# Optimization experiments

Measured on AMD Instinct MI355X. Metric: run time of the kernel, lower is better.

## Reference

```python
import jax, jax.numpy as jnp
import numpy as np
import math

D_MODEL = 512
N_HEAD = 8
TAU = 0.5


def _leaky_integrate(x):
    # dx/dt = -x / tau; x + dx/dt  (with tau=0.5 this equals -x)
    return x + (-x / TAU)


def setup_inputs() -> dict:
    key = jax.random.key(0)
    ks = jax.random.split(key, 12)
    B, S, D = 4, 2048, D_MODEL
    s = 1.0 / math.sqrt(D)
    inp = {
        "query": jax.random.normal(ks[0], (B, S, D), jnp.float32),
        "key": jax.random.normal(ks[1], (B, S, D), jnp.float32),
        "value": jax.random.normal(ks[2], (B, S, D), jnp.float32),
        "Wq": jax.random.normal(ks[3], (D, D), jnp.float32) * s,
        "bq": jnp.zeros((D,), jnp.float32),
        "Wk": jax.random.normal(ks[4], (D, D), jnp.float32) * s,
        "bk": jnp.zeros((D,), jnp.float32),
        "Wv": jax.random.normal(ks[5], (D, D), jnp.float32) * s,
        "bv": jnp.zeros((D,), jnp.float32),
        "Wo": jax.random.normal(ks[6], (D, D), jnp.float32) * s,
        "bo": jnp.zeros((D,), jnp.float32),
    }
    return inp


def reference(query, key, value, Wq, bq, Wk, bk, Wv, bv, Wo, bo):
    B, S, D = query.shape
    H = N_HEAD
    dh = D // H
    # linear projections (torch Linear: x @ W^T + b)
    q = query @ Wq.T + bq
    k = key @ Wk.T + bk
    v = value @ Wv.T + bv
    # (B, S, D) -> (B, H, S, dh)
    q = q.reshape(B, S, H, dh).transpose(0, 2, 1, 3)
    k = k.reshape(B, S, H, dh).transpose(0, 2, 1, 3)
    v = v.reshape(B, S, H, dh).transpose(0, 2, 1, 3)
    # leaky integration on q, k
    q = _leaky_integrate(q)
    k = _leaky_integrate(k)
    # scores scaled by sqrt(d_model) (NOT head dim) per the source
    scores = jnp.einsum("bhsd,bhtd->bhst", q, k) / math.sqrt(D_MODEL)
    attn = jax.nn.softmax(scores, axis=-1)
    # conductance-based synapse: elementwise sigmoid AFTER softmax
    attn = jax.nn.sigmoid(attn)
    out = jnp.einsum("bhst,bhtd->bhsd", attn, v)
    out = out.transpose(0, 2, 1, 3).reshape(B, S, D)
    return out @ Wo.T + bo
```

## Files before the change

kernel.cpp:

```cpp
#include <hip/hip_runtime.h>
#include <stdint.h>
#include <math.h>

using u16    = unsigned short;
using short8 = __attribute__((ext_vector_type(8))) short;
using f32x4  = __attribute__((ext_vector_type(4))) float;
using f32x16 = __attribute__((ext_vector_type(16))) float;
using u32x4  = __attribute__((ext_vector_type(4))) uint32_t;

#define DEVI __device__ __forceinline__
#define FENCE asm volatile("" ::: "memory")
#define GPTR(p) ((const __attribute__((address_space(1))) uint32_t*)(p))
#define LPTR(p) ((__attribute__((address_space(3))) uint32_t*)(p))

static constexpr int S  = 2048;
static constexpr int D  = 512;
static constexpr int DH = 64;
static constexpr float C2 = 0.063763906f;

DEVI u16 f2bf(float f){
  uint32_t u = __float_as_uint(f);
  u = u + 0x7FFFu + ((u >> 16) & 1u);
  return (u16)(u >> 16);
}

DEVI uint32_t cvt_pk_bf16(float a, float b){
  uint32_t d;
  asm("v_cvt_pk_bf16_f32 %0, %1, %2" : "=v"(d) : "v"(a), "v"(b));
  return d;
}

__global__ void k_cvt3(const float* __restrict__ a, const float* __restrict__ b,
                       const float* __restrict__ c, u16* __restrict__ out){
  int i = blockIdx.x * blockDim.x + threadIdx.x;
  const float* src = (i < (1<<20)) ? a : (i < (2<<20) ? b : c);
  float4 v = reinterpret_cast<const float4*>(src)[i & ((1<<20)-1)];
  uint2 o;
  o.x = (uint32_t)f2bf(v.x) | ((uint32_t)f2bf(v.y) << 16);
  o.y = (uint32_t)f2bf(v.z) | ((uint32_t)f2bf(v.w) << 16);
  reinterpret_cast<uint2*>(out)[i] = o;
}

__global__ void k_cvtw(const float* __restrict__ a, const float* __restrict__ b,
                       const float* __restrict__ c, const float* __restrict__ d,
                       u16* __restrict__ out){
  int i = blockIdx.x * blockDim.x + threadIdx.x;
  int sel = i >> 16;
  const float* src = sel == 0 ? a : sel == 1 ? b : sel == 2 ? c : d;
  float4 v = reinterpret_cast<const float4*>(src)[i & ((1<<16)-1)];
  uint2 o;
  o.x = (uint32_t)f2bf(v.x) | ((uint32_t)f2bf(v.y) << 16);
  o.y = (uint32_t)f2bf(v.z) | ((uint32_t)f2bf(v.w) << 16);
  reinterpret_cast<uint2*>(out)[i] = o;
}

template<int MODE>
__global__ __launch_bounds__(512)
void k_gemm_bt(const u16* __restrict__ A, const u16* __restrict__ W,
               const float* __restrict__ bias, void* __restrict__ outp, float oscale)
{
  __shared__ __align__(16) u16 As[2][128*64];
  __shared__ __align__(16) u16 Bs[2][128*64];
  const int tid = threadIdx.x;
  const int w = tid >> 6, l = tid & 63;
  const int wm = w & 3, wn = w >> 2;
  const int m0 = blockIdx.x * 128, n0 = blockIdx.y * 128;
  const int srow = l >> 3, sslot = l & 7;

  f32x4 acc[2][4];
  #pragma unroll
  for (int i = 0; i < 2; i++)
    #pragma unroll
    for (int j = 0; j < 4; j++)
      #pragma unroll
      for (int r = 0; r < 4; r++) acc[i][j][r] = 0.f;

  auto STAGE = [&](int buf, int kt){
    #pragma unroll
    for (int i = 0; i < 2; i++){
      int r = w*16 + i*8 + srow;
      int scol = (sslot ^ (r & 7)) * 8;
      long ga;
      if constexpr (MODE == 3){
        int m = m0 + r, k = kt + scol;
        ga = ((long)(((m >> 11)*8 + (k >> 6))*2048 + (m & 2047)))*64 + (k & 63);
      } else {
        ga = (long)(m0 + r)*D + kt + scol;
      }
      __builtin_amdgcn_global_load_lds(GPTR(A + ga), LPTR(&As[buf][(w*16 + i*8)*64]), 16, 0, 0);
      long gb = (long)(n0 + r)*D + kt + scol;
      __builtin_amdgcn_global_load_lds(GPTR(W + gb), LPTR(&Bs[buf][(w*16 + i*8)*64]), 16, 0, 0);
    }
  };

  STAGE(0, 0);
  asm volatile("s_waitcnt vmcnt(0)" ::: "memory");
  __builtin_amdgcn_s_barrier();
  FENCE;

  for (int kt = 0; kt < D; kt += 64){
    int buf = (kt >> 6) & 1;
    if (kt + 64 < D) STAGE(buf ^ 1, kt + 64);
    #pragma unroll
    for (int ks = 0; ks < 2; ks++){
      short8 af[2];
      #pragma unroll
      for (int mf = 0; mf < 2; mf++){
        int row = wm*32 + mf*16 + (l & 15);
        int cw = (ks*4 + (l >> 4)) ^ (row & 7);
        af[mf] = *reinterpret_cast<const short8*>(&As[buf][(row*8 + cw)*8]);
      }
      #pragma unroll
      for (int nf = 0; nf < 4; nf++){
        int row = wn*64 + nf*16 + (l & 15);
        int cw = (ks*4 + (l >> 4)) ^ (row & 7);
        short8 bf = *reinterpret_cast<const short8*>(&Bs[buf][(row*8 + cw)*8]);
        #pragma unroll
        for (int mf = 0; mf < 2; mf++)
          acc[mf][nf] = __builtin_amdgcn_mfma_f32_16x16x32_bf16(af[mf], bf, acc[mf][nf], 0, 0, 0);
      }
    }
    asm volatile("s_waitcnt vmcnt(0)" ::: "memory");
    __builtin_amdgcn_s_barrier();
    FENCE;
  }

  #pragma unroll
  for (int mf = 0; mf < 2; mf++){
    #pragma unroll
    for (int nf = 0; nf < 4; nf++){
      int n = n0 + wn*64 + nf*16 + (l & 15);
      float bi;
      if constexpr (MODE == 3) bi = bias[(m0 >> 11)*512 + n];
      else                     bi = bias[n];
      if constexpr (MODE == 2){
        int mb = m0 + wm*32 + mf*16 + (l >> 4)*4;
        int b_ = mb >> 11, s_ = mb & 2047;
        int h_ = n >> 6, d_ = n & 63;
        uint2 o;
        o.x = (uint32_t)f2bf((acc[mf][nf][0] + bi)*oscale) | ((uint32_t)f2bf((acc[mf][nf][1] + bi)*oscale) << 16);
        o.y = (uint32_t)f2bf((acc[mf][nf][2] + bi)*oscale) | ((uint32_t)f2bf((acc[mf][nf][3] + bi)*oscale) << 16);
        *reinterpret_cast<uint2*>(&((u16*)outp)[((long)((b_*8 + h_)*64 + d_))*2048 + s_]) = o;
      } else {
        #pragma unroll
        for (int r = 0; r < 4; r++){
          int m = m0 + wm*32 + mf*16 + (l >> 4)*4 + r;
          float v = (acc[mf][nf][r] + bi)*oscale;
          if constexpr (MODE == 3){
            ((float*)outp)[(long)m*D + n] = v;
          } else {
            int b_ = m >> 11, s_ = m & 2047;
            int h_ = n >> 6, d_ = n & 63;
            ((u16*)outp)[((long)((b_*8 + h_)*2048 + s_))*64 + d_] = f2bf(v);
          }
        }
      }
    }
  }
}

__global__ __launch_bounds__(256)
void k_sumv(const u16* __restrict__ Vt, float* __restrict__ SV){
  const int w = threadIdx.x >> 6, l = threadIdx.x & 63;
  const int row = blockIdx.x*4 + w;
  const u16* src = Vt + (long)row * S;
  float s = 0.f;
  #pragma unroll
  for (int j = 0; j < 4; j++){
    short8 v = *reinterpret_cast<const short8*>(&src[j*512 + l*8]);
    #pragma unroll
    for (int e = 0; e < 8; e++)
      s += __uint_as_float(((uint32_t)(u16)v[e]) << 16);
  }
  #pragma unroll
  for (int m = 1; m < 64; m <<= 1) s += __shfl_xor(s, m, 64);
  if (l == 0) SV[row] = s;
}

__global__ __launch_bounds__(256)
void k_bias2(const float* __restrict__ SV, const float* __restrict__ Wo,
             const float* __restrict__ bo, float* __restrict__ bias2){
  const int w = threadIdx.x >> 6, l = threadIdx.x & 63;
  const int idx = blockIdx.x*4 + w;
  const int b = idx >> 9, n = idx & 511;
  float dot = 0.f;
  #pragma unroll
  for (int j = 0; j < 2; j++){
    float4 wv = *reinterpret_cast<const float4*>(&Wo[(long)n*512 + l*8 + j*4]);
    float4 sv = *reinterpret_cast<const float4*>(&SV[b*512 + l*8 + j*4]);
    dot += wv.x*sv.x + wv.y*sv.y + wv.z*sv.z + wv.w*sv.w;
  }
  #pragma unroll
  for (int m = 1; m < 64; m <<= 1) dot += __shfl_xor(dot, m, 64);
  if (l == 0) bias2[idx] = bo[n] + 0.5f * dot;
}

__global__ __launch_bounds__(512, 4)
void k_flash(const u16* __restrict__ Qp, const u16* __restrict__ Kp,
             const u16* __restrict__ Vt, u16* __restrict__ AO)
{
  __shared__ __align__(16) u16 Ks[2][2][64*64];
  __shared__ __align__(16) u16 Vs[2][2][64*64];
  const int tid = threadIdx.x, w = tid >> 6, l = tid & 63;
  const int g = w >> 2, w4 = w & 3;
  const int bh = blockIdx.x & 31, qt = blockIdx.x >> 5;
  const u16* Qb = Qp + (long)bh * S * DH;
  const int hi = l >> 5, ln = l & 31;
  const int srow = l >> 3, sslot = l & 7;

  short8 qfr[4];
  #pragma unroll
  for (int c = 0; c < 4; c++){
    int row = qt*128 + w4*32 + ln;
    qfr[c] = *reinterpret_cast<const short8*>(&Qb[(long)row*DH + c*16 + hi*8]);
  }

  int koff[4], voff[8];
  #pragma unroll
  for (int c = 0; c < 4; c++)
    koff[c] = ln*64 + (((2*c + hi) ^ (ln & 7))*8);
  #pragma unroll
  for (int kf = 0; kf < 2; kf++)
    #pragma unroll
    for (int ch = 0; ch < 2; ch++)
      #pragma unroll
      for (int nf = 0; nf < 2; nf++)
        voff[kf*4 + ch*2 + nf] = (nf*32 + ln)*64 + ((((4*kf + 2*ch) + hi) ^ (ln & 7))*8);

  const u16* kptr = Kp + (long)bh*S*DH + g*4096;
  const u16* vptr = Vt + (long)bh*DH*S + g*64;
  long ksrc[2], vsrc[2];
  #pragma unroll
  for (int i = 0; i < 2; i++){
    int r = w4*16 + i*8 + srow;
    int sc = (sslot ^ (r & 7))*8;
    ksrc[i] = (long)r*64 + sc;
    vsrc[i] = (long)r*S + sc;
  }

  auto STAGE = [&](int buf){
    #pragma unroll
    for (int i = 0; i < 2; i++){
      __builtin_amdgcn_global_load_lds(GPTR(kptr + ksrc[i]), LPTR(&Ks[g][buf][(w4*16 + i*8)*64]), 16, 0, 0);
      __builtin_amdgcn_global_load_lds(GPTR(vptr + vsrc[i]), LPTR(&Vs[g][buf][(w4*16 + i*8)*64]), 16, 0, 0);
    }
    kptr += 8192;
    vptr += 128;
  };

  f32x16 oacc[2];
  #pragma unroll
  for (int j = 0; j < 2; j++)
    #pragma unroll
    for (int r = 0; r < 16; r++) oacc[j][r] = 0.f;
  float lsum = 0.f;

  STAGE(0);
  asm volatile("s_waitcnt vmcnt(0)" ::: "memory");
  __builtin_amdgcn_s_barrier();
  FENCE;

  const u16* KB = &Ks[g][0][0];
  const u16* VB = &Vs[g][0][0];

  for (int tp = 0; tp < 8; tp++){
    #pragma unroll
    for (int tt = 0; tt < 2; tt++){
      int t = tp*2 + tt;
      if (t < 15) STAGE(tt ^ 1);
      #pragma unroll
      for (int kf = 0; kf < 2; kf++){
        f32x16 sacc;
        #pragma unroll
        for (int r = 0; r < 16; r++) sacc[r] = 0.f;
        #pragma unroll
        for (int c = 0; c < 4; c++){
          short8 kfrag = *reinterpret_cast<const short8*>(KB + koff[c] + tt*4096 + kf*2048);
          sacc = __builtin_amdgcn_mfma_f32_32x32x16_bf16(kfrag, qfr[c], sacc, 0, 0, 0);
        }
        uint32_t pk[8];
        #pragma unroll
        for (int j = 0; j < 8; j++){
          float e0 = __builtin_amdgcn_exp2f(sacc[2*j]);
          float e1 = __builtin_amdgcn_exp2f(sacc[2*j+1]);
          lsum += e0 + e1;
          pk[j] = cvt_pk_bf16(e0, e1);
        }
        #pragma unroll
        for (int ch = 0; ch < 2; ch++){
          auto s1 = __builtin_amdgcn_permlane32_swap(pk[ch*4+0], pk[ch*4+2], false, false);
          auto s2 = __builtin_amdgcn_permlane32_swap(pk[ch*4+1], pk[ch*4+3], false, false);
          u32x4 av = { (uint32_t)s1[0], (uint32_t)s2[0], (uint32_t)s1[1], (uint32_t)s2[1] };
          short8 af = __builtin_bit_cast(short8, av);
          #pragma unroll
          for (int nf = 0; nf < 2; nf++){
            short8 vfrag = *reinterpret_cast<const short8*>(VB + voff[kf*4 + ch*2 + nf] + tt*4096);
            oacc[nf] = __builtin_amdgcn_mfma_f32_32x32x16_bf16(af, vfrag, oacc[nf], 0, 0, 0);
          }
        }
      }
      asm volatile("s_waitcnt vmcnt(0)" ::: "memory");
      __builtin_amdgcn_s_barrier();
      FENCE;
    }
  }

  lsum += __shfl_xor(lsum, 32, 64);
  float* OB = (float*)Ks;
  float* LB = (float*)Vs;
  if (g == 1){
    #pragma unroll
    for (int r = 0; r < 16; r++){
      int qrow = (r & 3) + 8*(r >> 2) + 4*hi;
      #pragma unroll
      for (int nf = 0; nf < 2; nf++)
        OB[w4*2048 + qrow*64 + nf*32 + ln] = oacc[nf][r];
    }
    if (hi == 0) LB[w4*32 + ln] = lsum;
  }
  __syncthreads();
  if (g == 0){
    float l2 = LB[w4*32 + ln];
    float linv = 0.25f / (lsum + l2);
    #pragma unroll
    for (int r = 0; r < 16; r++){
      int qrow = (r & 3) + 8*(r >> 2) + 4*hi;
      float sc = __shfl(linv, qrow, 64);
      int s_ = qt*128 + w4*32 + qrow;
      #pragma unroll
      for (int nf = 0; nf < 2; nf++){
        float o = oacc[nf][r] + OB[w4*2048 + qrow*64 + nf*32 + ln];
        AO[((long)bh*S + s_)*DH + nf*32 + ln] = f2bf(o * sc);
      }
    }
  }
}

extern "C" void kernel_launch(void* const* d_in, const int* in_sizes, int n_in,
                              void* d_out, int out_size, void* d_ws, size_t ws_size,
                              hipStream_t stream)
{
  const float* query = (const float*)d_in[0];
  const float* key_  = (const float*)d_in[1];
  const float* value = (const float*)d_in[2];
  const float* Wq = (const float*)d_in[3];
  const float* bq = (const float*)d_in[4];
  const float* Wk = (const float*)d_in[5];
  const float* bk = (const float*)d_in[6];
  const float* Wv = (const float*)d_in[7];
  const float* bv = (const float*)d_in[8];
  const float* Wo = (const float*)d_in[9];
  const float* bo = (const float*)d_in[10];

  char* ws = (char*)d_ws;
  const size_t XSZ = (size_t)8192 * 512 * 2;
  const size_t WSZ = (size_t)512 * 512 * 2;
  u16* xq  = (u16*)(ws);
  u16* xk  = (u16*)(ws + XSZ);
  u16* xv  = (u16*)(ws + 2*XSZ);
  u16* wqb = (u16*)(ws + 3*XSZ);
  u16* wkb = (u16*)(ws + 3*XSZ + WSZ);
  u16* wvb = (u16*)(ws + 3*XSZ + 2*WSZ);
  u16* wob = (u16*)(ws + 3*XSZ + 3*WSZ);
  u16* Qp  = (u16*)(ws + 3*XSZ + 4*WSZ);
  u16* Kp  = (u16*)(ws + 4*XSZ + 4*WSZ);
  u16* Vtp = (u16*)(ws + 5*XSZ + 4*WSZ);
  float* SV    = (float*)(ws + 6*XSZ + 4*WSZ);
  float* bias2 = (float*)(ws + 6*XSZ + 4*WSZ + 8192);
  u16* AO = xq;

  k_cvt3<<<(3<<20)/256, 256, 0, stream>>>(query, key_, value, xq);
  k_cvtw<<<(4<<16)/256, 256, 0, stream>>>(Wq, Wk, Wv, Wo, wqb);

  dim3 gg(64, 4), bb(512);
  k_gemm_bt<0><<<gg, bb, 0, stream>>>(xq, wqb, bq, (void*)Qp, C2);
  k_gemm_bt<0><<<gg, bb, 0, stream>>>(xk, wkb, bk, (void*)Kp, 1.0f);
  k_gemm_bt<2><<<gg, bb, 0, stream>>>(xv, wvb, bv, (void*)Vtp, 1.0f);

  k_sumv <<<512, 256, 0, stream>>>(Vtp, SV);
  k_bias2<<<512, 256, 0, stream>>>(SV, Wo, bo, bias2);

  k_flash<<<512, 512, 0, stream>>>(Qp, Kp, Vtp, AO);

  k_gemm_bt<3><<<gg, bb, 0, stream>>>(AO, wob, bias2, d_out, 1.0f);
}
```

Before: 110.1 us.

## Fuse fp32-to-bf16 input conversion into a single batched QKV projection GEMM

Removes the separate activation conversion kernel. The new QKV GEMM loads fp32 activations directly, converts them to bf16 in registers and writes them to LDS, while weights still arrive through direct global-to-LDS loads. The three projection launches are merged into one grid with a z dimension of 3. The flash kernel also adds s_setprio around its MFMA sections and seeds the first QK MFMA with a zero accumulator. The trade-off is that the A-operand path now goes through registers and needs extra VGPRs and LDS stores, and it reads twice the bytes from global memory.

```diff
diff --git a/kernel.cpp b/kernel.cpp
--- a/kernel.cpp
+++ b/kernel.cpp
@@ -28,17 +28,6 @@
   uint32_t d;
   asm("v_cvt_pk_bf16_f32 %0, %1, %2" : "=v"(d) : "v"(a), "v"(b));
   return d;
-}
-
-__global__ void k_cvt3(const float* __restrict__ a, const float* __restrict__ b,
-                       const float* __restrict__ c, u16* __restrict__ out){
-  int i = blockIdx.x * blockDim.x + threadIdx.x;
-  const float* src = (i < (1<<20)) ? a : (i < (2<<20) ? b : c);
-  float4 v = reinterpret_cast<const float4*>(src)[i & ((1<<20)-1)];
-  uint2 o;
-  o.x = (uint32_t)f2bf(v.x) | ((uint32_t)f2bf(v.y) << 16);
-  o.y = (uint32_t)f2bf(v.z) | ((uint32_t)f2bf(v.w) << 16);
-  reinterpret_cast<uint2*>(out)[i] = o;
 }
 
 __global__ void k_cvtw(const float* __restrict__ a, const float* __restrict__ b,
@@ -54,10 +43,128 @@
   reinterpret_cast<uint2*>(out)[i] = o;
 }
 
-template<int MODE>
 __global__ __launch_bounds__(512)
-void k_gemm_bt(const u16* __restrict__ A, const u16* __restrict__ W,
-               const float* __restrict__ bias, void* __restrict__ outp, float oscale)
+void k_gemm_qkv(const float* __restrict__ Xq, const float* __restrict__ Xk,
+                const float* __restrict__ Xv, const u16* __restrict__ Wall,
+                const float* __restrict__ bq, const float* __restrict__ bk,
+                const float* __restrict__ bv,
+                u16* __restrict__ Qp, u16* __restrict__ Kp, u16* __restrict__ Vtp)
+{
+  __shared__ __align__(16) u16 As[2][128*64];
+  __shared__ __align__(16) u16 Bs[2][128*64];
+  const int tid = threadIdx.x;
+  const int w = tid >> 6, l = tid & 63;
+  const int wm = w & 3, wn = w >> 2;
+  const int m0 = blockIdx.x * 128, n0 = blockIdx.y * 128;
+  const int z = blockIdx.z;
+  const int srow = l >> 3, sslot = l & 7;
+
+  const float* X = z == 0 ? Xq : (z == 1 ? Xk : Xv);
+  const u16*   W = Wall + (size_t)z * 512 * 512;
+  const float* bias = z == 0 ? bq : (z == 1 ? bk : bv);
+  const float oscale = z == 0 ? C2 : 1.0f;
+
+  const int arow = tid >> 2;
+  const int ac   = (tid & 3) * 16;
+
+  f32x4 acc[2][4];
+  #pragma unroll
+  for (int i = 0; i < 2; i++)
+    #pragma unroll
+    for (int j = 0; j < 4; j++)
+      #pragma unroll
+      for (int r = 0; r < 4; r++) acc[i][j][r] = 0.f;
+
+  float4 av[4];
+  auto LOADA = [&](int kt){
+    #pragma unroll
+    for (int j = 0; j < 4; j++)
+      av[j] = *reinterpret_cast<const float4*>(&X[(long)(m0 + arow)*D + kt + ac + j*4]);
+  };
+  auto WRITEA = [&](int buf){
+    #pragma unroll
+    for (int j2 = 0; j2 < 2; j2++){
+      u32x4 p;
+      p[0] = cvt_pk_bf16(av[2*j2].x,   av[2*j2].y);
+      p[1] = cvt_pk_bf16(av[2*j2].z,   av[2*j2].w);
+      p[2] = cvt_pk_bf16(av[2*j2+1].x, av[2*j2+1].y);
+      p[3] = cvt_pk_bf16(av[2*j2+1].z, av[2*j2+1].w);
+      int slot = ((ac >> 3) + j2) ^ (arow & 7);
+      *reinterpret_cast<u32x4*>(&As[buf][arow*64 + slot*8]) = p;
+    }
+  };
+  auto STAGEB = [&](int buf, int kt){
+    #pragma unroll
+    for (int i = 0; i < 2; i++){
+      int r = w*16 + i*8 + srow;
+      int scol = (sslot ^ (r & 7)) * 8;
+      __builtin_amdgcn_global_load_lds(GPTR(W + (long)(n0 + r)*D + kt + scol),
+                                       LPTR(&Bs[buf][(w*16 + i*8)*64]), 16, 0, 0);
+    }
+  };
+
+  LOADA(0); STAGEB(0, 0);
+  asm volatile("s_waitcnt vmcnt(0)" ::: "memory");
+  WRITEA(0);
+  __syncthreads();
+
+  for (int t = 0; t < 8; t++){
+    int buf = t & 1;
+    if (t < 7){ STAGEB(buf ^ 1, (t+1)*64); LOADA((t+1)*64); }
+    #pragma unroll
+    for (int ks = 0; ks < 2; ks++){
+      short8 af[2];
+      #pragma unroll
+      for (int mf = 0; mf < 2; mf++){
+        int row = wm*32 + mf*16 + (l & 15);
+        int cw = (ks*4 + (l >> 4)) ^ (row & 7);
+        af[mf] = *reinterpret_cast<const short8*>(&As[buf][(row*8 + cw)*8]);
+      }
+      #pragma unroll
+      for (int nf = 0; nf < 4; nf++){
+        int row = wn*64 + nf*16 + (l & 15);
+        int cw = (ks*4 + (l >> 4)) ^ (row & 7);
+        short8 bf = *reinterpret_cast<const short8*>(&Bs[buf][(row*8 + cw)*8]);
+        #pragma unroll
+        for (int mf = 0; mf < 2; mf++)
+          acc[mf][nf] = __builtin_amdgcn_mfma_f32_16x16x32_bf16(af[mf], bf, acc[mf][nf], 0, 0, 0);
+      }
+    }
+    asm volatile("s_waitcnt vmcnt(0)" ::: "memory");
+    if (t < 7) WRITEA(buf ^ 1);
+    __syncthreads();
+  }
+
+  #pragma unroll
+  for (int mf = 0; mf < 2; mf++){
+    #pragma unroll
+    for (int nf = 0; nf < 4; nf++){
+      int n = n0 + wn*64 + nf*16 + (l & 15);
+      float bi = bias[n];
+      int h_ = n >> 6, d_ = n & 63;
+      if (z == 2){
+        int mb = m0 + wm*32 + mf*16 + (l >> 4)*4;
+        int b_ = mb >> 11, s_ = mb & 2047;
+        uint2 o;
+        o.x = (uint32_t)f2bf(acc[mf][nf][0] + bi) | ((uint32_t)f2bf(acc[mf][nf][1] + bi) << 16);
+        o.y = (uint32_t)f2bf(acc[mf][nf][2] + bi) | ((uint32_t)f2bf(acc[mf][nf][3] + bi) << 16);
+        *reinterpret_cast<uint2*>(&Vtp[((long)((b_*8 + h_)*64 + d_))*2048 + s_]) = o;
+      } else {
+        u16* outp = z == 0 ? Qp : Kp;
+        #pragma unroll
+        for (int r = 0; r < 4; r++){
+          int m = m0 + wm*32 + mf*16 + (l >> 4)*4 + r;
+          int b_ = m >> 11, s_ = m & 2047;
+          outp[((long)((b_*8 + h_)*2048 + s_))*64 + d_] = f2bf((acc[mf][nf][r] + bi)*oscale);
+        }
+      }
+    }
+  }
+}
+
+__global__ __launch_bounds__(512)
+void k_gemm_ao(const u16* __restrict__ A, const u16* __restrict__ W,
+               const float* __restrict__ bias2, float* __restrict__ outp)
 {
   __shared__ __align__(16) u16 As[2][128*64];
   __shared__ __align__(16) u16 Bs[2][128*64];
@@ -80,13 +187,8 @@
     for (int i = 0; i < 2; i++){
       int r = w*16 + i*8 + srow;
       int scol = (sslot ^ (r & 7)) * 8;
-      long ga;
-      if constexpr (MODE == 3){
-        int m = m0 + r, k = kt + scol;
-        ga = ((long)(((m >> 11)*8 + (k >> 6))*2048 + (m & 2047)))*64 + (k & 63);
-      } else {
-        ga = (long)(m0 + r)*D + kt + scol;
-      }
+      int m = m0 + r, k = kt + scol;
+      long ga = ((long)(((m >> 11)*8 + (k >> 6))*2048 + (m & 2047)))*64 + (k & 63);
       __builtin_amdgcn_global_load_lds(GPTR(A + ga), LPTR(&As[buf][(w*16 + i*8)*64]), 16, 0, 0);
       long gb = (long)(n0 + r)*D + kt + scol;
       __builtin_amdgcn_global_load_lds(GPTR(W + gb), LPTR(&Bs[buf][(w*16 + i*8)*64]), 16, 0, 0);
@@ -126,37 +228,17 @@
   }
 
   #pragma unroll
-  for (int mf = 0; mf < 2; mf++){
+  for (int mf = 0; mf < 2; mf++)
     #pragma unroll
     for (int nf = 0; nf < 4; nf++){
       int n = n0 + wn*64 + nf*16 + (l & 15);
-      float bi;
-      if constexpr (MODE == 3) bi = bias[(m0 >> 11)*512 + n];
-      else                     bi = bias[n];
-      if constexpr (MODE == 2){
-        int mb = m0 + wm*32 + mf*16 + (l >> 4)*4;
-        int b_ = mb >> 11, s_ = mb & 2047;
-        int h_ = n >> 6, d_ = n & 63;
-        uint2 o;
-        o.x = (uint32_t)f2bf((acc[mf][nf][0] + bi)*oscale) | ((uint32_t)f2bf((acc[mf][nf][1] + bi)*oscale) << 16);
-        o.y = (uint32_t)f2bf((acc[mf][nf][2] + bi)*oscale) | ((uint32_t)f2bf((acc[mf][nf][3] + bi)*oscale) << 16);
-        *reinterpret_cast<uint2*>(&((u16*)outp)[((long)((b_*8 + h_)*64 + d_))*2048 + s_]) = o;
-      } else {
-        #pragma unroll
-        for (int r = 0; r < 4; r++){
-          int m = m0 + wm*32 + mf*16 + (l >> 4)*4 + r;
-          float v = (acc[mf][nf][r] + bi)*oscale;
-          if constexpr (MODE == 3){
-            ((float*)outp)[(long)m*D + n] = v;
-          } else {
-            int b_ = m >> 11, s_ = m & 2047;
-            int h_ = n >> 6, d_ = n & 63;
-            ((u16*)outp)[((long)((b_*8 + h_)*2048 + s_))*64 + d_] = f2bf(v);
-          }
-        }
-      }
-    }
-  }
+      float bi = bias2[(m0 >> 11)*512 + n];
+      #pragma unroll
+      for (int r = 0; r < 4; r++){
+        int m = m0 + wm*32 + mf*16 + (l >> 4)*4 + r;
+        outp[(long)m*D + n] = acc[mf][nf][r] + bi;
+      }
+    }
 }
 
 __global__ __launch_bounds__(256)
@@ -248,6 +330,9 @@
     vptr += 128;
   };
 
+  f32x16 zero16;
+  #pragma unroll
+  for (int r = 0; r < 16; r++) zero16[r] = 0.f;
   f32x16 oacc[2];
   #pragma unroll
   for (int j = 0; j < 2; j++)
@@ -270,14 +355,15 @@
       if (t < 15) STAGE(tt ^ 1);
       #pragma unroll
       for (int kf = 0; kf < 2; kf++){
-        f32x16 sacc;
-        #pragma unroll
-        for (int r = 0; r < 16; r++) sacc[r] = 0.f;
-        #pragma unroll
-        for (int c = 0; c < 4; c++){
+        __builtin_amdgcn_s_setprio(1);
+        short8 kf0 = *reinterpret_cast<const short8*>(KB + koff[0] + tt*4096 + kf*2048);
+        f32x16 sacc = __builtin_amdgcn_mfma_f32_32x32x16_bf16(kf0, qfr[0], zero16, 0, 0, 0);
+        #pragma unroll
+        for (int c = 1; c < 4; c++){
           short8 kfrag = *reinterpret_cast<const short8*>(KB + koff[c] + tt*4096 + kf*2048);
           sacc = __builtin_amdgcn_mfma_f32_32x32x16_bf16(kfrag, qfr[c], sacc, 0, 0, 0);
         }
+        __builtin_amdgcn_s_setprio(0);
         uint32_t pk[8];
         #pragma unroll
         for (int j = 0; j < 8; j++){
@@ -292,11 +378,13 @@
           auto s2 = __builtin_amdgcn_permlane32_swap(pk[ch*4+1], pk[ch*4+3], false, false);
           u32x4 av = { (uint32_t)s1[0], (uint32_t)s2[0], (uint32_t)s1[1], (uint32_t)s2[1] };
           short8 af = __builtin_bit_cast(short8, av);
+          __builtin_amdgcn_s_setprio(1);
           #pragma unroll
           for (int nf = 0; nf < 2; nf++){
             short8 vfrag = *reinterpret_cast<const short8*>(VB + voff[kf*4 + ch*2 + nf] + tt*4096);
             oacc[nf] = __builtin_amdgcn_mfma_f32_32x32x16_bf16(af, vfrag, oacc[nf], 0, 0, 0);
           }
+          __builtin_amdgcn_s_setprio(0);
         }
       }
       asm volatile("s_waitcnt vmcnt(0)" ::: "memory");
@@ -355,32 +443,25 @@
   char* ws = (char*)d_ws;
   const size_t XSZ = (size_t)8192 * 512 * 2;
   const size_t WSZ = (size_t)512 * 512 * 2;
-  u16* xq  = (u16*)(ws);
-  u16* xk  = (u16*)(ws + XSZ);
-  u16* xv  = (u16*)(ws + 2*XSZ);
-  u16* wqb = (u16*)(ws + 3*XSZ);
-  u16* wkb = (u16*)(ws + 3*XSZ + WSZ);
-  u16* wvb = (u16*)(ws + 3*XSZ + 2*WSZ);
-  u16* wob = (u16*)(ws + 3*XSZ + 3*WSZ);
-  u16* Qp  = (u16*)(ws + 3*XSZ + 4*WSZ);
-  u16* Kp  = (u16*)(ws + 4*XSZ + 4*WSZ);
-  u16* Vtp = (u16*)(ws + 5*XSZ + 4*WSZ);
-  float* SV    = (float*)(ws + 6*XSZ + 4*WSZ);
-  float* bias2 = (float*)(ws + 6*XSZ + 4*WSZ + 8192);
-  u16* AO = xq;
-
-  k_cvt3<<<(3<<20)/256, 256, 0, stream>>>(query, key_, value, xq);
+  u16* AO  = (u16*)(ws);
+  u16* wqb = (u16*)(ws + XSZ);
+  u16* wob = (u16*)(ws + XSZ + 3*WSZ);
+  u16* Qp  = (u16*)(ws + XSZ + 4*WSZ);
+  u16* Kp  = (u16*)(ws + 2*XSZ + 4*WSZ);
+  u16* Vtp = (u16*)(ws + 3*XSZ + 4*WSZ);
+  float* SV    = (float*)(ws + 4*XSZ + 4*WSZ);
+  float* bias2 = (float*)(ws + 4*XSZ + 4*WSZ + 8192);
+
   k_cvtw<<<(4<<16)/256, 256, 0, stream>>>(Wq, Wk, Wv, Wo, wqb);
 
-  dim3 gg(64, 4), bb(512);
-  k_gemm_bt<0><<<gg, bb, 0, stream>>>(xq, wqb, bq, (void*)Qp, C2);
-  k_gemm_bt<0><<<gg, bb, 0, stream>>>(xk, wkb, bk, (void*)Kp, 1.0f);
-  k_gemm_bt<2><<<gg, bb, 0, stream>>>(xv, wvb, bv, (void*)Vtp, 1.0f);
+  dim3 gq(64, 4, 3);
+  k_gemm_qkv<<<gq, 512, 0, stream>>>(query, key_, value, wqb, bq, bk, bv, Qp, Kp, Vtp);
 
   k_sumv <<<512, 256, 0, stream>>>(Vtp, SV);
   k_bias2<<<512, 256, 0, stream>>>(SV, Wo, bo, bias2);
 
   k_flash<<<512, 512, 0, stream>>>(Qp, Kp, Vtp, AO);
 
-  k_gemm_bt<3><<<gg, bb, 0, stream>>>(AO, wob, bias2, d_out, 1.0f);
-}
+  dim3 gg(64, 4);
+  k_gemm_ao<<<gg, 512, 0, stream>>>(AO, wob, bias2, (float*)d_out);
+}
```

Measured after the change: 98.22 us. 1.12x faster.
